# Optimization experiments

Hardware: AMD Instinct MI355X
Metric: run time of the kernel (lower is better)

## Reference

```python
import jax, jax.numpy as jnp
import numpy as np

KNN = 10        # knn init arg
FAC = 2.0       # fac init arg
SIGMA = 0.5     # self.sigma (fixed in module)
N, D = 4096, 128


def setup_inputs() -> dict:
    key = jax.random.key(0)
    k1, k2, k3 = jax.random.split(key, 3)
    return {
        "x": jax.random.normal(k1, (N, D), dtype=jnp.float32),
        "alpha": 0.01 * jax.random.normal(k2, (D,), dtype=jnp.float32),
        "base_noise": jax.random.normal(k3, (D,), dtype=jnp.float32),
    }


def _full_affinity_knn(Xm):
    r = jnp.sum(Xm * Xm, axis=1, keepdims=True)          # [N,1]
    Dx = r - 2.0 * (Xm @ Xm.T) + r.T                     # [N,N]
    # full row sort, take (knn-1)-th smallest distance per row
    sorted_d = jnp.sort(Dx, axis=1)                      # [N,N]
    knn_d = sorted_d[:, KNN - 1]                         # [N]
    # calculate_percentiles(percentile=50)
    s = jnp.sort(knn_d)
    n = s.shape[0]
    idx = int(50.0 / 100.0 * n)
    if n % 2 == 0:
        mu, ml = s[idx], s[idx - 1]
    else:
        mu = ml = s[idx]
    sigma = (mu + ml) / 2.0
    sigma = jnp.where(sigma < 1e-8, jnp.float32(1.0), sigma)
    W = jnp.exp(-Dx / (FAC * sigma))                     # [N,N]
    # Dminus @ W == row-normalize (diag matmul replaced by broadcast divide)
    P = W / jnp.sum(W, axis=1, keepdims=True)
    return P


def reference(x, alpha, base_noise):
    # feature_selector: hard_sigmoid(alpha + sigma*noise) applied per-feature
    z = alpha + SIGMA * base_noise
    gate = jnp.clip(z + 0.5, 0.0, 1.0)
    masked = x * gate[None, :]                           # [N,D]
    P = _full_affinity_knn(masked)                       # [N,N]
    return (P, masked)
```

## Files before the change

kernel.cpp:

```cpp
#include <hip/hip_runtime.h>
#include <math.h>

#define NROW 4096
#define NDIM 128
#define KNN 10
#define LDSS 136

typedef __bf16 bf16x8 __attribute__((ext_vector_type(8)));
typedef unsigned short u16x8 __attribute__((ext_vector_type(8)));
typedef unsigned short u16x4 __attribute__((ext_vector_type(4)));
typedef float f32x4 __attribute__((ext_vector_type(4)));

__device__ inline unsigned short f2bf(float f) {
    unsigned int u = __float_as_uint(f);
    u += 0x7FFFu + ((u >> 16) & 1u);
    return (unsigned short)(u >> 16);
}
__device__ inline float bf2f(unsigned short u) {
    return __uint_as_float((unsigned)u << 16);
}


__global__ __launch_bounds__(128) void k_mask(const float* __restrict__ x,
                                              const float* __restrict__ alpha,
                                              const float* __restrict__ noise,
                                              float* __restrict__ masked,
                                              unsigned short* __restrict__ mb,
                                              float* __restrict__ r) {
    int row = blockIdx.x;
    int c = threadIdx.x;
    float g = alpha[c] + 0.5f * noise[c] + 0.5f;
    g = fminf(fmaxf(g, 0.0f), 1.0f);
    float m = x[row * NDIM + c] * g;
    masked[row * NDIM + c] = m;
    mb[row * NDIM + c] = f2bf(m);
    float v = m * m;
#pragma unroll
    for (int o = 32; o > 0; o >>= 1) v += __shfl_down(v, o, 64);
    __shared__ float partial[2];
    if ((c & 63) == 0) partial[c >> 6] = v;
    __syncthreads();
    if (c == 0) r[row] = partial[0] + partial[1];
}

__global__ __launch_bounds__(256) void k_dx(const unsigned short* __restrict__ Mb,
                                            const float* __restrict__ r,
                                            float* __restrict__ P) {
    __shared__ __align__(16) __bf16 Asm[128 * LDSS];
    __shared__ __align__(16) __bf16 Bsm[128 * LDSS];
    int tid = threadIdx.x;
    int bx = blockIdx.x, by = blockIdx.y;

    {
        const unsigned short* Ap = Mb + (size_t)by * 128 * NDIM;
        const unsigned short* Bp = Mb + (size_t)bx * 128 * NDIM;
        int c = (tid & 15) * 8;
        int r0 = tid >> 4;
#pragma unroll
        for (int i = 0; i < 8; ++i) {
            int row = r0 + i * 16;
            *(uint4*)&Asm[row * LDSS + c] = *(const uint4*)(Ap + row * NDIM + c);
            *(uint4*)&Bsm[row * LDSS + c] = *(const uint4*)(Bp + row * NDIM + c);
        }
    }
    __syncthreads();

    int wave = tid >> 6, lane = tid & 63;
    int wr = wave >> 1, wc = wave & 1;
    int quad = lane >> 4, l15 = lane & 15;

    f32x4 acc[4][4];
#pragma unroll
    for (int i = 0; i < 4; ++i)
#pragma unroll
        for (int j = 0; j < 4; ++j) acc[i][j] = (f32x4)(0.0f);

#pragma unroll
    for (int kk = 0; kk < 128; kk += 32) {
        int ka = kk + quad * 8;
        bf16x8 af[4], bfr[4];
#pragma unroll
        for (int ti = 0; ti < 4; ++ti)
            af[ti] = *(const bf16x8*)&Asm[(wr * 64 + ti * 16 + l15) * LDSS + ka];
#pragma unroll
        for (int tj = 0; tj < 4; ++tj)
            bfr[tj] = *(const bf16x8*)&Bsm[(wc * 64 + tj * 16 + l15) * LDSS + ka];
#pragma unroll
        for (int ti = 0; ti < 4; ++ti)
#pragma unroll
            for (int tj = 0; tj < 4; ++tj)
                acc[ti][tj] = __builtin_amdgcn_mfma_f32_16x16x32_bf16(
                    af[ti], bfr[tj], acc[ti][tj], 0, 0, 0);
    }

    int gi_base = by * 128 + wr * 64;
    int gj_base = bx * 128 + wc * 64;
    float rrow[4][4], rcol[4];
#pragma unroll
    for (int ti = 0; ti < 4; ++ti)
#pragma unroll
        for (int rg = 0; rg < 4; ++rg)
            rrow[ti][rg] = r[gi_base + ti * 16 + quad * 4 + rg];
#pragma unroll
    for (int tj = 0; tj < 4; ++tj) rcol[tj] = r[gj_base + tj * 16 + l15];
#pragma unroll
    for (int ti = 0; ti < 4; ++ti)
#pragma unroll
        for (int rg = 0; rg < 4; ++rg) {
            int grow = gi_base + ti * 16 + quad * 4 + rg;
            __bf16* brow = (__bf16*)(P + (size_t)grow * NROW + NROW / 2);
#pragma unroll
            for (int tj = 0; tj < 4; ++tj) {
                int gcol = gj_base + tj * 16 + l15;
                float d = rrow[ti][rg] + rcol[tj] - 2.0f * acc[ti][tj][rg];
                ((unsigned short*)brow)[gcol] = f2bf(d);
            }
        }
}

__global__ __launch_bounds__(256) void k_knn(const float* __restrict__ P,
                                             float* __restrict__ knn) {
    int tid = threadIdx.x;
    int wave = tid >> 6, lane = tid & 63;
    int row = blockIdx.x * 4 + wave;
    const unsigned short* drow =
        (const unsigned short*)(P + (size_t)row * NROW + NROW / 2);

    u16x8 v8[8];
#pragma unroll
    for (int c = 0; c < 8; ++c)
        v8[c] = *(const u16x8*)(drow + (c * 64 + lane) * 8);

    float t[KNN];
#pragma unroll
    for (int j = 0; j < KNN; ++j) t[j] = INFINITY;

#pragma unroll
    for (int c = 0; c < 8; ++c) {
#pragma unroll
        for (int e = 0; e < 8; ++e) {
            float cv = bf2f(v8[c][e]);
            float t0n = fminf(t[0], cv);
#pragma unroll
            for (int j = KNN - 1; j >= 1; --j)
                t[j] = __builtin_amdgcn_fmed3f(cv, t[j - 1], t[j]);
            t[0] = t0n;
        }
    }

#pragma unroll
    for (int r = 0; r < KNN; ++r) {
        float m = t[0];
#pragma unroll
        for (int o = 1; o < 64; o <<= 1)
            m = fminf(m, __shfl_xor(m, o, 64));
        if (r == KNN - 1) {
            if (lane == 0) knn[row] = m;
        } else {
            unsigned long long mask = __ballot(t[0] == m);
            if (lane == (int)(__ffsll((unsigned long long)mask) - 1)) {
#pragma unroll
                for (int j = 0; j < KNN - 1; ++j) t[j] = t[j + 1];
                t[KNN - 1] = INFINITY;
            }
        }
    }
}

__device__ inline unsigned fmap(float f) {
    unsigned b = __float_as_uint(f);
    return b ^ ((b >> 31) ? 0xFFFFFFFFu : 0x80000000u);
}
__device__ inline float funmap(unsigned u) {
    unsigned b = (u & 0x80000000u) ? (u ^ 0x80000000u) : ~u;
    return __uint_as_float(b);
}

__global__ __launch_bounds__(1024) void k_sigma(const float* __restrict__ knn,
                                                float* __restrict__ scale_out) {
    __shared__ unsigned keys[NROW];
    __shared__ unsigned hist[2048];
    __shared__ unsigned s_prefix, s_R;
    __shared__ unsigned red_lo[16], red_hi[16];
    __shared__ float red_f[16];
    __shared__ unsigned red_u[16];
    int tid = threadIdx.x;
    int lane = tid & 63, wid = tid >> 6;

    unsigned kmin = 0xFFFFFFFFu, kmax = 0u;
#pragma unroll
    for (int l = 0; l < 4; ++l) {
        unsigned k = fmap(knn[tid + l * 1024]);
        keys[tid + l * 1024] = k;
        kmin = min(kmin, k);
        kmax = max(kmax, k);
    }
#pragma unroll
    for (int o = 32; o > 0; o >>= 1) {
        kmin = min(kmin, (unsigned)__shfl_down(kmin, o, 64));
        kmax = max(kmax, (unsigned)__shfl_down(kmax, o, 64));
    }
    if (lane == 0) { red_lo[wid] = kmin; red_hi[wid] = kmax; }
    __syncthreads();
    kmin = red_lo[0]; kmax = red_hi[0];
#pragma unroll
    for (int w = 1; w < 16; ++w) {
        kmin = min(kmin, red_lo[w]);
        kmax = max(kmax, red_hi[w]);
    }

    unsigned xr = kmin ^ kmax;
    int B = (xr == 0u) ? 0 : (32 - __builtin_clz(xr));
    unsigned prefix0 = (B >= 32) ? 0u : (kmin >> B);

    if (tid == 0) { s_prefix = prefix0; s_R = 2047; }
    __syncthreads();

    int rem = B;
    for (int rd = 0; rd < 3; ++rd) {
        int w = rem > 11 ? 11 : rem;
        int sh = rem - w;
        unsigned nb = 1u << w;
        hist[tid] = 0;
        hist[tid + 1024] = 0;
        __syncthreads();
        unsigned prefix = s_prefix;
        unsigned R = s_R;
        int hsh = rem;
#pragma unroll
        for (int l = 0; l < 4; ++l) {
            unsigned k = keys[tid + l * 1024];
            bool match = (rd == 0) || ((k >> hsh) == prefix);
            if (match) atomicAdd(&hist[(k >> sh) & (nb - 1u)], 1u);
        }
        __syncthreads();
        if (tid < 64) {
            unsigned chunk = (nb >= 64u) ? (nb >> 6) : 1u;
            unsigned base = tid * chunk;
            unsigned lsum = 0;
            if (base < nb)
                for (unsigned i = 0; i < chunk; ++i) lsum += hist[base + i];
            unsigned pfx = lsum;
#pragma unroll
            for (int o = 1; o < 64; o <<= 1) {
                unsigned v = __shfl_up(pfx, o, 64);
                if (tid >= o) pfx += v;
            }
            unsigned excl = pfx - lsum;
            if (R >= excl && R < excl + lsum) {
                unsigned cum = excl;
                for (unsigned i = 0; i < chunk; ++i) {
                    unsigned h = hist[base + i];
                    if (R < cum + h) {
                        s_prefix = (prefix << w) | (base + i);
                        s_R = R - cum;
                        break;
                    }
                    cum += h;
                }
            }
        }
        __syncthreads();
        rem = sh;
    }

    unsigned mlk = s_prefix;
    unsigned cnt = 0, mng = 0xFFFFFFFFu;
#pragma unroll
    for (int l = 0; l < 4; ++l) {
        unsigned k = keys[tid + l * 1024];
        if (k <= mlk) cnt++;
        else mng = min(mng, k);
    }
#pragma unroll
    for (int o = 32; o > 0; o >>= 1) {
        cnt += __shfl_down(cnt, o, 64);
        mng = min(mng, (unsigned)__shfl_down(mng, o, 64));
    }
    if (lane == 0) { red_u[wid] = cnt; red_f[wid] = __uint_as_float(mng); }
    __syncthreads();
    if (tid == 0) {
        unsigned ctot = 0, m = 0xFFFFFFFFu;
        for (int w = 0; w < 16; ++w) {
            ctot += red_u[w];
            m = min(m, __float_as_uint(red_f[w]));
        }
        float ml = funmap(mlk);
        float mu = (ctot >= 2049u) ? ml : funmap(m);
        float sigma = 0.5f * (mu + ml);
        if (sigma < 1e-8f) sigma = 1.0f;
        scale_out[0] = -1.0f / (2.0f * sigma);
    }
}

__global__ __launch_bounds__(256) void k_norm(float* __restrict__ P,
                                              const float* __restrict__ scale_p) {
    int row = blockIdx.x, tid = threadIdx.x;
    float scale = scale_p[0];
    float* drow = P + (size_t)row * NROW;
    const unsigned short* brow = (const unsigned short*)(drow + NROW / 2);

    u16x4 a[4];
#pragma unroll
    for (int j = 0; j < 4; ++j)
        a[j] = *(const u16x4*)(brow + (j * 256 + tid) * 4);

    float v[16];
#pragma unroll
    for (int j = 0; j < 4; ++j)
#pragma unroll
        for (int e = 0; e < 4; ++e)
            v[j * 4 + e] = __expf(bf2f(a[j][e]) * scale);

    float sum = 0.0f;
#pragma unroll
    for (int e = 0; e < 16; ++e) sum += v[e];
#pragma unroll
    for (int o = 32; o > 0; o >>= 1) sum += __shfl_down(sum, o, 64);
    __shared__ float ps[4];
    int lane = tid & 63, wid = tid >> 6;
    if (lane == 0) ps[wid] = sum;
    __syncthreads();
    float inv = 1.0f / (ps[0] + ps[1] + ps[2] + ps[3]);
#pragma unroll
    for (int j = 0; j < 4; ++j) {
        float4 o4;
        o4.x = v[j * 4 + 0] * inv;
        o4.y = v[j * 4 + 1] * inv;
        o4.z = v[j * 4 + 2] * inv;
        o4.w = v[j * 4 + 3] * inv;
        *(float4*)(drow + (j * 256 + tid) * 4) = o4;
    }
}

extern "C" void kernel_launch(void* const* d_in, const int* in_sizes, int n_in,
                              void* d_out, int out_size, void* d_ws, size_t ws_size,
                              hipStream_t stream) {
    const float* x = (const float*)d_in[0];
    const float* alpha = (const float*)d_in[1];
    const float* noise = (const float*)d_in[2];
    float* out = (float*)d_out;
    float* P = out;
    float* masked = out + (size_t)NROW * NROW;
    float* ws = (float*)d_ws;
    float* r = ws;
    float* knn = ws + NROW;
    float* scale = ws + 2 * NROW;
    unsigned short* Mb = (unsigned short*)(ws + 3 * NROW);

    k_mask<<<NROW, 128, 0, stream>>>(x, alpha, noise, masked, Mb, r);
    k_dx<<<dim3(NROW / 128, NROW / 128), 256, 0, stream>>>(Mb, r, P);
    k_knn<<<NROW / 4, 256, 0, stream>>>(P, knn);
    k_sigma<<<1, 1024, 0, stream>>>(knn, scale);
    k_norm<<<NROW, 256, 0, stream>>>(P, scale);
}
```

Before: 124.9 us.

## Move bf16 distances to workspace and split kNN row across four waves

The bf16 distance matrix moves from the upper half of each output row in P to a separate workspace buffer, so k_norm no longer reads and writes the same rows. k_knn now gives each row to a whole 256-thread block: each of the four waves keeps a per-lane top-K over a quarter of the row, then wave 0 merges the four per-wave top-10 lists through shared memory. This gives each lane less serial med3 insertion work and launches four times as many blocks, at the cost of an extra merge step and a block barrier. The workspace must be large enough to hold the 32 MB bf16 matrix.

```diff
diff --git a/kernel.cpp b/kernel.cpp
--- a/kernel.cpp
+++ b/kernel.cpp
@@ -45,7 +45,7 @@
 
 __global__ __launch_bounds__(256) void k_dx(const unsigned short* __restrict__ Mb,
                                             const float* __restrict__ r,
-                                            float* __restrict__ P) {
+                                            unsigned short* __restrict__ Dxb) {
     __shared__ __align__(16) __bf16 Asm[128 * LDSS];
     __shared__ __align__(16) __bf16 Bsm[128 * LDSS];
     int tid = threadIdx.x;
@@ -108,27 +108,26 @@
 #pragma unroll
         for (int rg = 0; rg < 4; ++rg) {
             int grow = gi_base + ti * 16 + quad * 4 + rg;
-            __bf16* brow = (__bf16*)(P + (size_t)grow * NROW + NROW / 2);
+            unsigned short* brow = Dxb + (size_t)grow * NROW;
 #pragma unroll
             for (int tj = 0; tj < 4; ++tj) {
                 int gcol = gj_base + tj * 16 + l15;
                 float d = rrow[ti][rg] + rcol[tj] - 2.0f * acc[ti][tj][rg];
-                ((unsigned short*)brow)[gcol] = f2bf(d);
+                brow[gcol] = f2bf(d);
             }
         }
 }
 
-__global__ __launch_bounds__(256) void k_knn(const float* __restrict__ P,
+__global__ __launch_bounds__(256) void k_knn(const unsigned short* __restrict__ Dxb,
                                              float* __restrict__ knn) {
     int tid = threadIdx.x;
     int wave = tid >> 6, lane = tid & 63;
-    int row = blockIdx.x * 4 + wave;
-    const unsigned short* drow =
-        (const unsigned short*)(P + (size_t)row * NROW + NROW / 2);
-
-    u16x8 v8[8];
-#pragma unroll
-    for (int c = 0; c < 8; ++c)
+    int row = blockIdx.x;
+    const unsigned short* drow = Dxb + (size_t)row * NROW + wave * 1024;
+
+    u16x8 v8[2];
+#pragma unroll
+    for (int c = 0; c < 2; ++c)
         v8[c] = *(const u16x8*)(drow + (c * 64 + lane) * 8);
 
     float t[KNN];
@@ -136,7 +135,7 @@
     for (int j = 0; j < KNN; ++j) t[j] = INFINITY;
 
 #pragma unroll
-    for (int c = 0; c < 8; ++c) {
+    for (int c = 0; c < 2; ++c)
 #pragma unroll
         for (int e = 0; e < 8; ++e) {
             float cv = bf2f(v8[c][e]);
@@ -146,22 +145,37 @@
                 t[j] = __builtin_amdgcn_fmed3f(cv, t[j - 1], t[j]);
             t[0] = t0n;
         }
-    }
-
+
+    __shared__ float wtop[4 * KNN];
 #pragma unroll
     for (int r = 0; r < KNN; ++r) {
         float m = t[0];
 #pragma unroll
         for (int o = 1; o < 64; o <<= 1)
             m = fminf(m, __shfl_xor(m, o, 64));
-        if (r == KNN - 1) {
-            if (lane == 0) knn[row] = m;
-        } else {
-            unsigned long long mask = __ballot(t[0] == m);
-            if (lane == (int)(__ffsll((unsigned long long)mask) - 1)) {
-#pragma unroll
-                for (int j = 0; j < KNN - 1; ++j) t[j] = t[j + 1];
-                t[KNN - 1] = INFINITY;
+        if (lane == 0) wtop[wave * KNN + r] = m;
+        unsigned long long mask = __ballot(t[0] == m);
+        if (lane == (int)(__ffsll((long long)mask) - 1)) {
+#pragma unroll
+            for (int j = 0; j < KNN - 1; ++j) t[j] = t[j + 1];
+            t[KNN - 1] = INFINITY;
+        }
+    }
+    __syncthreads();
+
+    if (wave == 0) {
+        float val = (lane < 4 * KNN) ? wtop[lane] : INFINITY;
+#pragma unroll
+        for (int r = 0; r < KNN; ++r) {
+            float m = val;
+#pragma unroll
+            for (int o = 1; o < 64; o <<= 1)
+                m = fminf(m, __shfl_xor(m, o, 64));
+            if (r == KNN - 1) {
+                if (lane == 0) knn[row] = m;
+            } else {
+                unsigned long long mask = __ballot(val == m);
+                if (lane == (int)(__ffsll((long long)mask) - 1)) val = INFINITY;
             }
         }
     }
@@ -293,12 +307,13 @@
     }
 }
 
-__global__ __launch_bounds__(256) void k_norm(float* __restrict__ P,
+__global__ __launch_bounds__(256) void k_norm(const unsigned short* __restrict__ Dxb,
+                                              float* __restrict__ P,
                                               const float* __restrict__ scale_p) {
     int row = blockIdx.x, tid = threadIdx.x;
     float scale = scale_p[0];
     float* drow = P + (size_t)row * NROW;
-    const unsigned short* brow = (const unsigned short*)(drow + NROW / 2);
+    const unsigned short* brow = Dxb + (size_t)row * NROW;
 
     u16x4 a[4];
 #pragma unroll
@@ -347,10 +362,11 @@
     float* knn = ws + NROW;
     float* scale = ws + 2 * NROW;
     unsigned short* Mb = (unsigned short*)(ws + 3 * NROW);
+    unsigned short* Dxb = Mb + (size_t)NROW * NDIM;
 
     k_mask<<<NROW, 128, 0, stream>>>(x, alpha, noise, masked, Mb, r);
-    k_dx<<<dim3(NROW / 128, NROW / 128), 256, 0, stream>>>(Mb, r, P);
-    k_knn<<<NROW / 4, 256, 0, stream>>>(P, knn);
+    k_dx<<<dim3(NROW / 128, NROW / 128), 256, 0, stream>>>(Mb, r, Dxb);
+    k_knn<<<NROW, 256, 0, stream>>>(Dxb, knn);
     k_sigma<<<1, 1024, 0, stream>>>(knn, scale);
-    k_norm<<<NROW, 256, 0, stream>>>(P, scale);
-}
+    k_norm<<<NROW, 256, 0, stream>>>(Dxb, P, scale);
+}
```

Measured after the change: 132.6 us. 6.2% more time.

## Spread each kNN row across a full block with shared-memory tree merge

Applied to the files above, without the earlier changes.

The kNN selection kernel now assigns one row per 256-thread block instead of one row per wave. Each thread keeps a top-10 list over 16 elements instead of 64, and the per-thread lists are merged through a shared-memory tree reduction with block barriers, replacing the wave-level min-extraction loop. This shortens each thread's serial insertion chain and launches four times as many blocks. In exchange it adds eight synchronized merge rounds with heavy LDS traffic, and threads that drop out of the tree sit idle.

```diff
diff --git a/kernel.cpp b/kernel.cpp
--- a/kernel.cpp
+++ b/kernel.cpp
@@ -122,13 +122,13 @@
                                              float* __restrict__ knn) {
     int tid = threadIdx.x;
     int wave = tid >> 6, lane = tid & 63;
-    int row = blockIdx.x * 4 + wave;
+    int row = blockIdx.x;
     const unsigned short* drow =
-        (const unsigned short*)(P + (size_t)row * NROW + NROW / 2);
-
-    u16x8 v8[8];
-#pragma unroll
-    for (int c = 0; c < 8; ++c)
+        (const unsigned short*)(P + (size_t)row * NROW + NROW / 2) + wave * 1024;
+
+    u16x8 v8[2];
+#pragma unroll
+    for (int c = 0; c < 2; ++c)
         v8[c] = *(const u16x8*)(drow + (c * 64 + lane) * 8);
 
     float t[KNN];
@@ -136,7 +136,7 @@
     for (int j = 0; j < KNN; ++j) t[j] = INFINITY;
 
 #pragma unroll
-    for (int c = 0; c < 8; ++c) {
+    for (int c = 0; c < 2; ++c)
 #pragma unroll
         for (int e = 0; e < 8; ++e) {
             float cv = bf2f(v8[c][e]);
@@ -146,25 +146,32 @@
                 t[j] = __builtin_amdgcn_fmed3f(cv, t[j - 1], t[j]);
             t[0] = t0n;
         }
-    }
-
-#pragma unroll
-    for (int r = 0; r < KNN; ++r) {
-        float m = t[0];
-#pragma unroll
-        for (int o = 1; o < 64; o <<= 1)
-            m = fminf(m, __shfl_xor(m, o, 64));
-        if (r == KNN - 1) {
-            if (lane == 0) knn[row] = m;
-        } else {
-            unsigned long long mask = __ballot(t[0] == m);
-            if (lane == (int)(__ffsll((unsigned long long)mask) - 1)) {
-#pragma unroll
-                for (int j = 0; j < KNN - 1; ++j) t[j] = t[j + 1];
-                t[KNN - 1] = INFINITY;
-            }
-        }
-    }
+
+    __shared__ float M[256][KNN + 1];
+#pragma unroll
+    for (int j = 0; j < KNN; ++j) M[tid][j] = t[j];
+    __syncthreads();
+
+#pragma unroll
+    for (int s = 128; s >= 1; s >>= 1) {
+        if (tid < s) {
+#pragma unroll
+            for (int i = 0; i < KNN; ++i) {
+                float cv = M[tid + s][i];
+                float t0n = fminf(t[0], cv);
+#pragma unroll
+                for (int j = KNN - 1; j >= 1; --j)
+                    t[j] = __builtin_amdgcn_fmed3f(cv, t[j - 1], t[j]);
+                t[0] = t0n;
+            }
+            if (s > 1) {
+#pragma unroll
+                for (int j = 0; j < KNN; ++j) M[tid][j] = t[j];
+            }
+        }
+        __syncthreads();
+    }
+    if (tid == 0) knn[row] = t[KNN - 1];
 }
 
 __device__ inline unsigned fmap(float f) {
@@ -350,7 +357,7 @@
 
     k_mask<<<NROW, 128, 0, stream>>>(x, alpha, noise, masked, Mb, r);
     k_dx<<<dim3(NROW / 128, NROW / 128), 256, 0, stream>>>(Mb, r, P);
-    k_knn<<<NROW / 4, 256, 0, stream>>>(P, knn);
+    k_knn<<<NROW, 256, 0, stream>>>(P, knn);
     k_sigma<<<1, 1024, 0, stream>>>(knn, scale);
     k_norm<<<NROW, 256, 0, stream>>>(P, scale);
 }
```

Result: slower. 128.8 us (+3.1%).
